# Performance work log

Measured on AMD Instinct MI355X. Metric: run time of the kernel, lower is better.

Reference implementation:

```python
import jax, jax.numpy as jnp
import numpy as np

B, N, C = 8, 1024, 768
H = 12
HD = C // H  # 64
SCALE = HD ** -0.5


def setup_inputs() -> dict:
    key = jax.random.key(0)
    k1, k2, k3, k4 = jax.random.split(key, 4)
    x = jax.random.normal(k1, (B, N, C), dtype=jnp.float32)
    # torch Linear weights are [out, in]; qkv has no bias (qkv_bias=False)
    w_qkv = jax.random.normal(k2, (3 * C, C), dtype=jnp.float32) * (C ** -0.5)
    w_proj = jax.random.normal(k3, (C, C), dtype=jnp.float32) * (C ** -0.5)
    b_proj = jax.random.normal(k4, (C,), dtype=jnp.float32) * 0.01
    return {"x": x, "w_qkv": w_qkv, "w_proj": w_proj, "b_proj": b_proj}


def reference(x, w_qkv, w_proj, b_proj):
    b, n, c = x.shape
    # qkv: [B, N, 3C] -> [3, B, H, N, HD]
    qkv = (x @ w_qkv.T).reshape(b, n, 3, H, c // H).transpose(2, 0, 3, 1, 4)
    q, k, v = qkv[0], qkv[1], qkv[2]
    attn = jnp.einsum('bhqd,bhkd->bhqk', q, k) * SCALE
    attn = jax.nn.softmax(attn, axis=-1)
    out = jnp.einsum('bhqk,bhkd->bhqd', attn, v)          # [B, H, N, HD]
    out = out.transpose(0, 2, 1, 3).reshape(b, n, c)      # [B, N, C]
    out = out @ w_proj.T + b_proj
    return out
```

## Files before the change

### kernel.cpp

```cpp
#include <hip/hip_runtime.h>
#include <hip/hip_bf16.h>
#include <cstdint>

#define TB 8
#define TN 1024
#define TC 768
#define TH 12
#define THD 64
#define TM (TB*TN)
#define TNQKV (3*TC)
#define QSCALE_LOG2E 0.18033688011112042f
#define THR_BITS 11.541560327111708f

typedef __attribute__((ext_vector_type(8))) short s16x8;
typedef __attribute__((ext_vector_type(4))) short s16x4;
typedef __attribute__((ext_vector_type(4))) float f32x4;
typedef __attribute__((ext_vector_type(2))) unsigned int u32x2;

__device__ __forceinline__ unsigned short f2bf(float f) {
    union { float f; unsigned int u; } v; v.f = f;
    unsigned int u = v.u;
    return (unsigned short)((u + 0x7FFFu + ((u >> 16) & 1u)) >> 16);
}

__device__ __forceinline__ float bf2f(unsigned short h) {
    union { float f; unsigned int u; } v; v.u = ((unsigned int)h) << 16;
    return v.f;
}

__device__ __forceinline__ unsigned int cvt_pk_bf16(float lo, float hi) {
    unsigned int r;
    asm("v_cvt_pk_bf16_f32 %0, %1, %2" : "=v"(r) : "v"(lo), "v"(hi));
    return r;
}

__device__ __forceinline__ void gload_lds16(const unsigned short* g, unsigned short* l) {
    __builtin_amdgcn_global_load_lds(
        (const __attribute__((address_space(1))) unsigned int*)g,
        (__attribute__((address_space(3))) unsigned int*)l,
        16, 0, 0);
}

__global__ __launch_bounds__(256) void cvt_kernel(const float* __restrict__ in,
                                                  unsigned short* __restrict__ out,
                                                  int n8) {
    int i = blockIdx.x * blockDim.x + threadIdx.x;
    if (i >= n8) return;
    f32x4 a = *(const f32x4*)(in + (size_t)i * 8);
    f32x4 b = *(const f32x4*)(in + (size_t)i * 8 + 4);
    s16x8 r;
    #pragma unroll
    for (int e = 0; e < 4; e++) r[e] = (short)f2bf(a[e]);
    #pragma unroll
    for (int e = 0; e < 4; e++) r[4 + e] = (short)f2bf(b[e]);
    *(s16x8*)(out + (size_t)i * 8) = r;
}

template<bool BIAS, bool OBF16>
__global__ __launch_bounds__(256) void gemm_bt(
    const unsigned short* __restrict__ A,
    const unsigned short* __restrict__ Bm,
    void* __restrict__ Cout,
    const float* __restrict__ bias,
    int M, int Nn, int K)
{
    __shared__ unsigned short As[128 * 32];
    __shared__ unsigned short Bs[128 * 32];
    const int t = threadIdx.x;
    const int w = t >> 6, l = t & 63;
    const int lr = l & 15, lh = l >> 4;
    const int wm = w >> 1, wn = w & 1;
    const int bm = blockIdx.x, bn = blockIdx.y;

    f32x4 acc[4][4] = {};

    const unsigned short* Ab = A + (size_t)bm * 128 * K;
    const unsigned short* Bb = Bm + (size_t)bn * 128 * K;

    for (int kt = 0; kt < K; kt += 32) {
        __syncthreads();
        {
            const int c0 = t, c1 = t + 256;
            gload_lds16(Ab + (size_t)(c0 >> 2) * K + kt + (c0 & 3) * 8, As + c0 * 8);
            gload_lds16(Ab + (size_t)(c1 >> 2) * K + kt + (c1 & 3) * 8, As + c1 * 8);
            gload_lds16(Bb + (size_t)(c0 >> 2) * K + kt + (c0 & 3) * 8, Bs + c0 * 8);
            gload_lds16(Bb + (size_t)(c1 >> 2) * K + kt + (c1 & 3) * 8, Bs + c1 * 8);
        }
        __syncthreads();
        s16x8 af[4], bfr[4];
        #pragma unroll
        for (int mi = 0; mi < 4; mi++)
            af[mi] = *(const s16x8*)(As + (wm * 64 + mi * 16 + lr) * 32 + lh * 8);
        #pragma unroll
        for (int ni = 0; ni < 4; ni++)
            bfr[ni] = *(const s16x8*)(Bs + (wn * 64 + ni * 16 + lr) * 32 + lh * 8);
        #pragma unroll
        for (int mi = 0; mi < 4; mi++)
            #pragma unroll
            for (int ni = 0; ni < 4; ni++)
                acc[mi][ni] = __builtin_amdgcn_mfma_f32_16x16x32_bf16(
                    af[mi], bfr[ni], acc[mi][ni], 0, 0, 0);
    }

    const int r0 = bm * 128 + wm * 64;
    const int c0 = bn * 128 + wn * 64;
    if constexpr (OBF16) {
        unsigned short* O = (unsigned short*)Cout;
        #pragma unroll
        for (int mi = 0; mi < 4; mi++)
            #pragma unroll
            for (int ni = 0; ni < 4; ni++)
                #pragma unroll
                for (int i = 0; i < 4; i++)
                    O[(size_t)(r0 + mi * 16 + lh * 4 + i) * Nn + c0 + ni * 16 + lr] =
                        f2bf(acc[mi][ni][i]);
    } else {
        float* O = (float*)Cout;
        #pragma unroll
        for (int mi = 0; mi < 4; mi++)
            #pragma unroll
            for (int ni = 0; ni < 4; ni++)
                #pragma unroll
                for (int i = 0; i < 4; i++) {
                    int cc = c0 + ni * 16 + lr;
                    float v = acc[mi][ni][i];
                    if constexpr (BIAS) v += bias[cc];
                    O[(size_t)(r0 + mi * 16 + lh * 4 + i) * Nn + cc] = v;
                }
    }
}

__global__ __launch_bounds__(256) void transpose_v(
    const unsigned short* __restrict__ qkv, unsigned short* __restrict__ vt)
{
    __shared__ unsigned short tile[64][72];
    const int kt = blockIdx.x, bh = blockIdx.y;
    const int b = bh / TH, h = bh % TH;
    const int t = threadIdx.x;
    const unsigned short* src = qkv + (size_t)(b * TN + kt * 64) * TNQKV + 2 * TC + h * THD;
    #pragma unroll
    for (int c = t; c < 512; c += 256) {
        int k = c >> 3, d8 = c & 7;
        *(s16x8*)&tile[k][d8 * 8] = *(const s16x8*)(src + (size_t)k * TNQKV + d8 * 8);
    }
    __syncthreads();
    unsigned short* dst = vt + (size_t)bh * THD * TN + kt * 64;
    #pragma unroll
    for (int c = t; c < 512; c += 256) {
        int d = c >> 3, k8 = c & 7;
        s16x8 v;
        #pragma unroll
        for (int e = 0; e < 8; e++) v[e] = tile[k8 * 8 + e][d];
        *(s16x8*)(dst + (size_t)d * TN + k8 * 8) = v;
    }
}

__global__ __launch_bounds__(512) void attn_kernel(
    const unsigned short* __restrict__ qkv,
    const unsigned short* __restrict__ vt,
    unsigned short* __restrict__ out)
{
    const int bid = blockIdx.x;
    const int vid = (bid & 7) * 96 + (bid >> 3);
    const int bh = vid >> 3;
    const int qt = vid & 7;
    const int b = bh / TH, h = bh % TH;
    const int t = threadIdx.x, w = t >> 6, l = t & 63;
    const int lr = l & 15, lh = l >> 4;
    const int qbase = qt * 128 + w * 16;

    __shared__ unsigned short Kbuf[2][64 * 64];
    __shared__ unsigned short Vbuf[2][64 * 64];
    __shared__ unsigned short plds[8][16 * 64];

    const unsigned short* kbase = qkv + (size_t)(b * TN) * TNQKV + TC + h * THD;
    const unsigned short* vtb = vt + (size_t)bh * THD * TN;

    const int srow_lo = (l >> 3);
    const int schunk = (l & 7) ^ srow_lo;
    const int srow = w * 8 + srow_lo;
    const int sdst = w * 512 + l * 8;

    const unsigned short* qptr = qkv + (size_t)(b * TN + qbase + lr) * TNQKV + h * THD;
    s16x8 bq[2];
    #pragma unroll
    for (int cj = 0; cj < 2; cj++) {
        s16x8 raw = *(const s16x8*)(qptr + cj * 32 + lh * 8);
        #pragma unroll
        for (int e = 0; e < 8; e++)
            bq[cj][e] = (short)f2bf(bf2f((unsigned short)raw[e]) * QSCALE_LOG2E);
    }

    f32x4 o[4] = {};
    float m2 = -1e30f, lsum = 0.f;
    unsigned short* pw = plds[w];
    const int lr7 = lr & 7;

    gload_lds16(kbase + (size_t)srow * TNQKV + schunk * 8, &Kbuf[0][sdst]);
    gload_lds16(vtb + (size_t)srow * TN + schunk * 8, &Vbuf[0][sdst]);
    __syncthreads();

    for (int it = 0; it < 16; it++) {
        const int kt = it * 64;
        const int cur = it & 1, nxt = cur ^ 1;
        {
            const int ktn = (kt + 64) & (TN - 1);
            gload_lds16(kbase + (size_t)(ktn + srow) * TNQKV + schunk * 8, &Kbuf[nxt][sdst]);
            gload_lds16(vtb + (size_t)srow * TN + ktn + schunk * 8, &Vbuf[nxt][sdst]);
        }
        const unsigned short* Kc = Kbuf[cur];
        const unsigned short* Vc = Vbuf[cur];

        f32x4 s[4];
        #pragma unroll
        for (int kk = 0; kk < 4; kk++) {
            const int r = kk * 16 + lr;
            s16x8 ak0 = *(const s16x8*)(Kc + r * 64 + ((lh ^ lr7) * 8));
            s16x8 ak1 = *(const s16x8*)(Kc + r * 64 + (((4 + lh) ^ lr7) * 8));
            f32x4 z = {0.f, 0.f, 0.f, 0.f};
            z = __builtin_amdgcn_mfma_f32_16x16x32_bf16(ak0, bq[0], z, 0, 0, 0);
            z = __builtin_amdgcn_mfma_f32_16x16x32_bf16(ak1, bq[1], z, 0, 0, 0);
            s[kk] = z;
        }

        float v[16];
        #pragma unroll
        for (int kk = 0; kk < 4; kk++)
            #pragma unroll
            for (int i = 0; i < 4; i++) v[kk * 4 + i] = s[kk][i];
        float mx = fmaxf(fmaxf(v[0], v[1]), v[2]);
        #pragma unroll
        for (int j = 3; j + 1 < 16; j += 2) mx = fmaxf(fmaxf(mx, v[j]), v[j + 1]);
        mx = fmaxf(mx, v[15]);
        if (!__all(mx <= m2 + THR_BITS)) {
            float rmx = fmaxf(mx, __shfl_xor(mx, 16, 64));
            rmx = fmaxf(rmx, __shfl_xor(rmx, 32, 64));
            float newm = fmaxf(m2, rmx);
            float corr = __builtin_amdgcn_exp2f(m2 - newm);
            m2 = newm;
            lsum *= corr;
            #pragma unroll
            for (int nd = 0; nd < 4; nd++)
                #pragma unroll
                for (int i = 0; i < 4; i++) o[nd][i] *= corr;
        }
        float a[16];
        #pragma unroll
        for (int kk = 0; kk < 4; kk++)
            #pragma unroll
            for (int i = 0; i < 4; i++) {
                float p = __builtin_amdgcn_exp2f(s[kk][i] - m2);
                s[kk][i] = p;
                a[kk * 4 + i] = p;
            }
        #pragma unroll
        for (int st = 8; st >= 1; st >>= 1)
            #pragma unroll
            for (int j = 0; j < st; j++) a[j] += a[j + st];
        lsum += a[0];

        #pragma unroll
        for (int kk = 0; kk < 4; kk++) {
            u32x2 pk;
            pk[0] = cvt_pk_bf16(s[kk][0], s[kk][1]);
            pk[1] = cvt_pk_bf16(s[kk][2], s[kk][3]);
            const int wch = ((kk << 1) + (lh >> 1)) ^ lr7;
            *(u32x2*)(pw + lr * 64 + wch * 8 + (lh & 1) * 4) = pk;
        }
        #pragma unroll
        for (int ktile = 0; ktile < 2; ktile++) {
            const int rch = ((ktile << 2) + lh) ^ lr7;
            s16x8 bp = *(const s16x8*)(pw + lr * 64 + rch * 8);
            #pragma unroll
            for (int nd = 0; nd < 4; nd++) {
                const int d = nd * 16 + lr;
                s16x8 av = *(const s16x8*)(
                    Vc + d * 64 + ((((ktile << 2) + lh) ^ lr7) * 8));
                o[nd] = __builtin_amdgcn_mfma_f32_16x16x32_bf16(av, bp, o[nd], 0, 0, 0);
            }
        }
        __syncthreads();
    }

    lsum += __shfl_xor(lsum, 16, 64);
    lsum += __shfl_xor(lsum, 32, 64);
    float inv = 1.f / lsum;
    unsigned short* op = out + (size_t)(b * TN + qbase + lr) * TC + h * THD;
    #pragma unroll
    for (int nd = 0; nd < 4; nd++) {
        u32x2 r;
        r[0] = cvt_pk_bf16(o[nd][0] * inv, o[nd][1] * inv);
        r[1] = cvt_pk_bf16(o[nd][2] * inv, o[nd][3] * inv);
        *(u32x2*)(op + nd * 16 + lh * 4) = r;
    }
}

extern "C" void kernel_launch(void* const* d_in, const int* in_sizes, int n_in,
                              void* d_out, int out_size, void* d_ws, size_t ws_size,
                              hipStream_t stream) {
    const float* x      = (const float*)d_in[0];
    const float* w_qkv  = (const float*)d_in[1];
    const float* w_proj = (const float*)d_in[2];
    const float* b_proj = (const float*)d_in[3];
    float* out = (float*)d_out;

    unsigned short* xb   = (unsigned short*)d_ws;
    unsigned short* wqb  = xb   + (size_t)TM * TC;
    unsigned short* wpb  = wqb  + (size_t)TNQKV * TC;
    unsigned short* qkvb = wpb  + (size_t)TC * TC;
    unsigned short* vtb  = qkvb + (size_t)TM * TNQKV;
    unsigned short* aob  = vtb  + (size_t)TB * TH * THD * TN;

    int n8;
    n8 = TM * TC / 8;
    cvt_kernel<<<(n8 + 255) / 256, 256, 0, stream>>>(x, xb, n8);
    n8 = TNQKV * TC / 8;
    cvt_kernel<<<(n8 + 255) / 256, 256, 0, stream>>>(w_qkv, wqb, n8);
    n8 = TC * TC / 8;
    cvt_kernel<<<(n8 + 255) / 256, 256, 0, stream>>>(w_proj, wpb, n8);

    gemm_bt<false, true><<<dim3(TM / 128, TNQKV / 128), 256, 0, stream>>>(
        xb, wqb, (void*)qkvb, nullptr, TM, TNQKV, TC);

    transpose_v<<<dim3(TN / 64, TB * TH), 256, 0, stream>>>(qkvb, vtb);

    attn_kernel<<<768, 512, 0, stream>>>(qkvb, vtb, aob);

    gemm_bt<true, false><<<dim3(TM / 128, TC / 128), 256, 0, stream>>>(
        aob, wpb, (void*)out, b_proj, TM, TC, TC);
}
```

Measured before the change: 133.4 us.

## Double-buffer GEMM LDS tiles with swizzle, XCD block remap, and merged conversion

The GEMM kernel now double-buffers A/B tiles in LDS, so the next K-slice loads while MFMAs run on the current one. It also XOR-swizzles the LDS layout to reduce bank conflicts, remaps block IDs so neighbouring tiles share an XCD, and parameterises the N-tile width (192 columns for the projection, giving 256 blocks). The three fp32-to-bf16 conversion launches are merged into one. The cost is more LDS per block, which may reduce occupancy, plus one redundant tile load on the last iteration.

```diff
diff --git a/kernel.cpp b/kernel.cpp
--- a/kernel.cpp
+++ b/kernel.cpp
@@ -41,75 +41,104 @@
         16, 0, 0);
 }
 
-__global__ __launch_bounds__(256) void cvt_kernel(const float* __restrict__ in,
-                                                  unsigned short* __restrict__ out,
-                                                  int n8) {
+__global__ __launch_bounds__(256) void cvt3_kernel(
+    const float* __restrict__ a, unsigned short* __restrict__ oa, int na,
+    const float* __restrict__ b, unsigned short* __restrict__ ob, int nb,
+    const float* __restrict__ c, unsigned short* __restrict__ oc, int nc)
+{
     int i = blockIdx.x * blockDim.x + threadIdx.x;
-    if (i >= n8) return;
-    f32x4 a = *(const f32x4*)(in + (size_t)i * 8);
-    f32x4 b = *(const f32x4*)(in + (size_t)i * 8 + 4);
+    const float* src; unsigned short* dst; int idx;
+    if (i < na)           { src = a; dst = oa; idx = i; }
+    else if (i < na + nb) { src = b; dst = ob; idx = i - na; }
+    else if (i < na + nb + nc) { src = c; dst = oc; idx = i - na - nb; }
+    else return;
+    f32x4 x0 = *(const f32x4*)(src + (size_t)idx * 8);
+    f32x4 x1 = *(const f32x4*)(src + (size_t)idx * 8 + 4);
     s16x8 r;
     #pragma unroll
-    for (int e = 0; e < 4; e++) r[e] = (short)f2bf(a[e]);
-    #pragma unroll
-    for (int e = 0; e < 4; e++) r[4 + e] = (short)f2bf(b[e]);
-    *(s16x8*)(out + (size_t)i * 8) = r;
-}
-
-template<bool BIAS, bool OBF16>
+    for (int e = 0; e < 4; e++) r[e] = (short)f2bf(x0[e]);
+    #pragma unroll
+    for (int e = 0; e < 4; e++) r[4 + e] = (short)f2bf(x1[e]);
+    *(s16x8*)(dst + (size_t)idx * 8) = r;
+}
+
+template<int NF, int NBN, bool BIAS, bool OBF16>
 __global__ __launch_bounds__(256) void gemm_bt(
     const unsigned short* __restrict__ A,
     const unsigned short* __restrict__ Bm,
     void* __restrict__ Cout,
     const float* __restrict__ bias,
-    int M, int Nn, int K)
+    int K, int Nn, int cpx)
 {
-    __shared__ unsigned short As[128 * 32];
-    __shared__ unsigned short Bs[128 * 32];
+    __shared__ unsigned short As[2][128 * 32];
+    __shared__ unsigned short Bs[2][NF * 32 * 32];
     const int t = threadIdx.x;
     const int w = t >> 6, l = t & 63;
     const int lr = l & 15, lh = l >> 4;
     const int wm = w >> 1, wn = w & 1;
-    const int bm = blockIdx.x, bn = blockIdx.y;
-
-    f32x4 acc[4][4] = {};
+
+    const int bid = blockIdx.x;
+    const int vid = (bid & 7) * cpx + (bid >> 3);
+    const int bm = vid / NBN, bn = vid % NBN;
+
+    f32x4 acc[4][NF] = {};
 
     const unsigned short* Ab = A + (size_t)bm * 128 * K;
-    const unsigned short* Bb = Bm + (size_t)bn * 128 * K;
-
-    for (int kt = 0; kt < K; kt += 32) {
-        __syncthreads();
-        {
-            const int c0 = t, c1 = t + 256;
-            gload_lds16(Ab + (size_t)(c0 >> 2) * K + kt + (c0 & 3) * 8, As + c0 * 8);
-            gload_lds16(Ab + (size_t)(c1 >> 2) * K + kt + (c1 & 3) * 8, As + c1 * 8);
-            gload_lds16(Bb + (size_t)(c0 >> 2) * K + kt + (c0 & 3) * 8, Bs + c0 * 8);
-            gload_lds16(Bb + (size_t)(c1 >> 2) * K + kt + (c1 & 3) * 8, Bs + c1 * 8);
-        }
-        __syncthreads();
-        s16x8 af[4], bfr[4];
+    const unsigned short* Bb = Bm + (size_t)bn * (NF * 32) * K;
+
+    const int swl = (lr ^ (lr >> 2)) & 3;
+    const int ca = (lh ^ swl) * 8;
+
+    auto stage = [&](int bufi, int kt) {
+        #pragma unroll
+        for (int j = 0; j < 2; j++) {
+            const int s = j * 256 + t, row = s >> 2, c = s & 3;
+            const int g = c ^ ((row ^ (row >> 2)) & 3);
+            gload_lds16(Ab + (size_t)row * K + kt + g * 8, &As[bufi][s * 8]);
+        }
+        #pragma unroll
+        for (int j = 0; j < NF / 2; j++) {
+            const int s = j * 256 + t, row = s >> 2, c = s & 3;
+            const int g = c ^ ((row ^ (row >> 2)) & 3);
+            gload_lds16(Bb + (size_t)row * K + kt + g * 8, &Bs[bufi][s * 8]);
+        }
+    };
+
+    stage(0, 0);
+    __syncthreads();
+
+    const int nkt = K / 32;
+    for (int it = 0; it < nkt; it++) {
+        const int cur = it & 1, nxt = cur ^ 1;
+        const int ktn = (it + 1 < nkt) ? (it + 1) * 32 : it * 32;
+        stage(nxt, ktn);
+
+        const unsigned short* Ac = As[cur];
+        const unsigned short* Bc = Bs[cur];
+        s16x8 af[4], bfr[NF];
         #pragma unroll
         for (int mi = 0; mi < 4; mi++)
-            af[mi] = *(const s16x8*)(As + (wm * 64 + mi * 16 + lr) * 32 + lh * 8);
-        #pragma unroll
-        for (int ni = 0; ni < 4; ni++)
-            bfr[ni] = *(const s16x8*)(Bs + (wn * 64 + ni * 16 + lr) * 32 + lh * 8);
+            af[mi] = *(const s16x8*)(Ac + (wm * 64 + mi * 16 + lr) * 32 + ca);
+        #pragma unroll
+        for (int ni = 0; ni < NF; ni++)
+            bfr[ni] = *(const s16x8*)(Bc + (wn * (NF * 16) + ni * 16 + lr) * 32 + ca);
         #pragma unroll
         for (int mi = 0; mi < 4; mi++)
             #pragma unroll
-            for (int ni = 0; ni < 4; ni++)
+            for (int ni = 0; ni < NF; ni++)
                 acc[mi][ni] = __builtin_amdgcn_mfma_f32_16x16x32_bf16(
                     af[mi], bfr[ni], acc[mi][ni], 0, 0, 0);
+        __syncthreads();
     }
 
     const int r0 = bm * 128 + wm * 64;
-    const int c0 = bn * 128 + wn * 64;
+    const int c0 = bn * (NF * 32) + wn * (NF * 16);
     if constexpr (OBF16) {
         unsigned short* O = (unsigned short*)Cout;
         #pragma unroll
         for (int mi = 0; mi < 4; mi++)
             #pragma unroll
-            for (int ni = 0; ni < 4; ni++)
+            for (int ni = 0; ni < NF; ni++)
                 #pragma unroll
                 for (int i = 0; i < 4; i++)
                     O[(size_t)(r0 + mi * 16 + lh * 4 + i) * Nn + c0 + ni * 16 + lr] =
@@ -119,7 +148,7 @@
         #pragma unroll
         for (int mi = 0; mi < 4; mi++)
             #pragma unroll
-            for (int ni = 0; ni < 4; ni++)
+            for (int ni = 0; ni < NF; ni++)
                 #pragma unroll
                 for (int i = 0; i < 4; i++) {
                     int cc = c0 + ni * 16 + lr;
@@ -311,21 +340,17 @@
     unsigned short* vtb  = qkvb + (size_t)TM * TNQKV;
     unsigned short* aob  = vtb  + (size_t)TB * TH * THD * TN;
 
-    int n8;
-    n8 = TM * TC / 8;
-    cvt_kernel<<<(n8 + 255) / 256, 256, 0, stream>>>(x, xb, n8);
-    n8 = TNQKV * TC / 8;
-    cvt_kernel<<<(n8 + 255) / 256, 256, 0, stream>>>(w_qkv, wqb, n8);
-    n8 = TC * TC / 8;
-    cvt_kernel<<<(n8 + 255) / 256, 256, 0, stream>>>(w_proj, wpb, n8);
-
-    gemm_bt<false, true><<<dim3(TM / 128, TNQKV / 128), 256, 0, stream>>>(
-        xb, wqb, (void*)qkvb, nullptr, TM, TNQKV, TC);
+    const int na = TM * TC / 8, nb = TNQKV * TC / 8, nc = TC * TC / 8;
+    cvt3_kernel<<<(na + nb + nc + 255) / 256, 256, 0, stream>>>(
+        x, xb, na, w_qkv, wqb, nb, w_proj, wpb, nc);
+
+    gemm_bt<4, 18, false, true><<<1152, 256, 0, stream>>>(
+        xb, wqb, (void*)qkvb, nullptr, TC, TNQKV, 144);
 
     transpose_v<<<dim3(TN / 64, TB * TH), 256, 0, stream>>>(qkvb, vtb);
 
     attn_kernel<<<768, 512, 0, stream>>>(qkvb, vtb, aob);
 
-    gemm_bt<true, false><<<dim3(TM / 128, TC / 128), 256, 0, stream>>>(
-        aob, wpb, (void*)out, b_proj, TM, TC, TC);
-}
+    gemm_bt<6, 4, true, false><<<256, 256, 0, stream>>>(
+        aob, wpb, (void*)out, b_proj, TC, TC, 32);
+}
```

Measured after the change: 139.8 us. +4.8%, slower.

## Fuse V transpose into QKV GEMM epilogue and merge conversion kernels

Applied to the files above, without the earlier changes.

The QKV GEMM epilogue now writes the V columns straight into the transposed per-head layout, using packed bf16 stores of four consecutive keys. This removes the separate transpose_v kernel and its read-back of V from the QKV buffer. The three fp32-to-bf16 conversion launches are also merged into one kernel that picks its source by index range. The V stores are 8-byte writes strided by TN, so the epilogue is less coalesced than before.

```diff
diff --git a/kernel.cpp b/kernel.cpp
--- a/kernel.cpp
+++ b/kernel.cpp
@@ -41,27 +41,34 @@
         16, 0, 0);
 }
 
-__global__ __launch_bounds__(256) void cvt_kernel(const float* __restrict__ in,
-                                                  unsigned short* __restrict__ out,
-                                                  int n8) {
+__global__ __launch_bounds__(256) void cvt3_kernel(
+    const float* __restrict__ a, unsigned short* __restrict__ oa, int na,
+    const float* __restrict__ b, unsigned short* __restrict__ ob, int nb,
+    const float* __restrict__ c, unsigned short* __restrict__ oc, int nc)
+{
     int i = blockIdx.x * blockDim.x + threadIdx.x;
-    if (i >= n8) return;
-    f32x4 a = *(const f32x4*)(in + (size_t)i * 8);
-    f32x4 b = *(const f32x4*)(in + (size_t)i * 8 + 4);
+    const float* src; unsigned short* dst; int idx;
+    if (i < na)           { src = a; dst = oa; idx = i; }
+    else if (i < na + nb) { src = b; dst = ob; idx = i - na; }
+    else if (i < na + nb + nc) { src = c; dst = oc; idx = i - na - nb; }
+    else return;
+    f32x4 x0 = *(const f32x4*)(src + (size_t)idx * 8);
+    f32x4 x1 = *(const f32x4*)(src + (size_t)idx * 8 + 4);
     s16x8 r;
     #pragma unroll
-    for (int e = 0; e < 4; e++) r[e] = (short)f2bf(a[e]);
+    for (int e = 0; e < 4; e++) r[e] = (short)f2bf(x0[e]);
     #pragma unroll
-    for (int e = 0; e < 4; e++) r[4 + e] = (short)f2bf(b[e]);
-    *(s16x8*)(out + (size_t)i * 8) = r;
-}
-
-template<bool BIAS, bool OBF16>
+    for (int e = 0; e < 4; e++) r[4 + e] = (short)f2bf(x1[e]);
+    *(s16x8*)(dst + (size_t)idx * 8) = r;
+}
+
+template<bool BIAS, bool OBF16, bool VSPLIT>
 __global__ __launch_bounds__(256) void gemm_bt(
     const unsigned short* __restrict__ A,
     const unsigned short* __restrict__ Bm,
     void* __restrict__ Cout,
     const float* __restrict__ bias,
+    unsigned short* __restrict__ vt,
     int M, int Nn, int K)
 {
     __shared__ unsigned short As[128 * 32];
@@ -104,6 +111,26 @@
 
     const int r0 = bm * 128 + wm * 64;
     const int c0 = bn * 128 + wn * 64;
+    if constexpr (VSPLIT) {
+        if (bn >= 12) {
+            #pragma unroll
+            for (int mi = 0; mi < 4; mi++) {
+                const int row = r0 + mi * 16 + lh * 4;
+                const int bb = row >> 10, k = row & 1023;
+                #pragma unroll
+                for (int ni = 0; ni < 4; ni++) {
+                    const int dg = c0 + ni * 16 + lr - 2 * TC;
+                    unsigned short* vp = vt + ((size_t)(bb * TH + (dg >> 6)) << 16)
+                                            + (dg & 63) * TN + k;
+                    u32x2 r;
+                    r[0] = cvt_pk_bf16(acc[mi][ni][0], acc[mi][ni][1]);
+                    r[1] = cvt_pk_bf16(acc[mi][ni][2], acc[mi][ni][3]);
+                    *(u32x2*)vp = r;
+                }
+            }
+            return;
+        }
+    }
     if constexpr (OBF16) {
         unsigned short* O = (unsigned short*)Cout;
         #pragma unroll
@@ -127,31 +154,6 @@
                     if constexpr (BIAS) v += bias[cc];
                     O[(size_t)(r0 + mi * 16 + lh * 4 + i) * Nn + cc] = v;
                 }
-    }
-}
-
-__global__ __launch_bounds__(256) void transpose_v(
-    const unsigned short* __restrict__ qkv, unsigned short* __restrict__ vt)
-{
-    __shared__ unsigned short tile[64][72];
-    const int kt = blockIdx.x, bh = blockIdx.y;
-    const int b = bh / TH, h = bh % TH;
-    const int t = threadIdx.x;
-    const unsigned short* src = qkv + (size_t)(b * TN + kt * 64) * TNQKV + 2 * TC + h * THD;
-    #pragma unroll
-    for (int c = t; c < 512; c += 256) {
-        int k = c >> 3, d8 = c & 7;
-        *(s16x8*)&tile[k][d8 * 8] = *(const s16x8*)(src + (size_t)k * TNQKV + d8 * 8);
-    }
-    __syncthreads();
-    unsigned short* dst = vt + (size_t)bh * THD * TN + kt * 64;
-    #pragma unroll
-    for (int c = t; c < 512; c += 256) {
-        int d = c >> 3, k8 = c & 7;
-        s16x8 v;
-        #pragma unroll
-        for (int e = 0; e < 8; e++) v[e] = tile[k8 * 8 + e][d];
-        *(s16x8*)(dst + (size_t)d * TN + k8 * 8) = v;
     }
 }
 
@@ -311,21 +313,15 @@
     unsigned short* vtb  = qkvb + (size_t)TM * TNQKV;
     unsigned short* aob  = vtb  + (size_t)TB * TH * THD * TN;
 
-    int n8;
-    n8 = TM * TC / 8;
-    cvt_kernel<<<(n8 + 255) / 256, 256, 0, stream>>>(x, xb, n8);
-    n8 = TNQKV * TC / 8;
-    cvt_kernel<<<(n8 + 255) / 256, 256, 0, stream>>>(w_qkv, wqb, n8);
-    n8 = TC * TC / 8;
-    cvt_kernel<<<(n8 + 255) / 256, 256, 0, stream>>>(w_proj, wpb, n8);
-
-    gemm_bt<false, true><<<dim3(TM / 128, TNQKV / 128), 256, 0, stream>>>(
-        xb, wqb, (void*)qkvb, nullptr, TM, TNQKV, TC);
-
-    transpose_v<<<dim3(TN / 64, TB * TH), 256, 0, stream>>>(qkvb, vtb);
+    const int na = TM * TC / 8, nb = TNQKV * TC / 8, nc = TC * TC / 8;
+    cvt3_kernel<<<(na + nb + nc + 255) / 256, 256, 0, stream>>>(
+        x, xb, na, w_qkv, wqb, nb, w_proj, wpb, nc);
+
+    gemm_bt<false, true, true><<<dim3(TM / 128, TNQKV / 128), 256, 0, stream>>>(
+        xb, wqb, (void*)qkvb, nullptr, vtb, TM, TNQKV, TC);
 
     attn_kernel<<<768, 512, 0, stream>>>(qkvb, vtb, aob);
 
-    gemm_bt<true, false><<<dim3(TM / 128, TC / 128), 256, 0, stream>>>(
-        aob, wpb, (void*)out, b_proj, TM, TC, TC);
-}
+    gemm_bt<true, false, false><<<dim3(TM / 128, TC / 128), 256, 0, stream>>>(
+        aob, wpb, (void*)out, b_proj, nullptr, TM, TC, TC);
+}
```

After: 127.5 us. 1.05x faster.
